# Performance work log

Hardware: AMD Instinct MI355X
Metric: run time of the kernel (lower is better)

## Reference

```python
import jax, jax.numpy as jnp
import numpy as np

N, E = 50000, 800000
IN_DIM, H0, H1, OUT_DIM = 64, 64, 64, 8
NUM_RELS, NUM_BASES = 16, 8


def setup_inputs() -> dict:
    key = jax.random.key(0)
    ks = jax.random.split(key, 20)
    features = jax.random.normal(ks[0], (N, IN_DIM), dtype=jnp.float32)
    etypes = jax.random.randint(ks[1], (E,), 0, NUM_RELS)
    src = jax.random.randint(ks[2], (E,), 0, N)
    dst = jax.random.randint(ks[3], (E,), 0, N)
    # degree normalization 1/in_degree(dst), as DGL stores in g.edata['norm']
    deg = jax.ops.segment_sum(jnp.ones((E,), jnp.float32), dst, num_segments=N)
    norm = (1.0 / jnp.maximum(deg, 1.0))[dst][:, None]  # [E,1]

    def glorot(k, shape):
        fan_in, fan_out = shape[-2], shape[-1]
        lim = jnp.sqrt(6.0 / (fan_in + fan_out)).astype(jnp.float32)
        return jax.random.uniform(k, shape, jnp.float32, -lim, lim)

    dims = [(IN_DIM, H0), (H0, H1), (H1, OUT_DIM)]
    inp = {"features": features, "norm": norm}
    for i, (di, do) in enumerate(dims):
        inp[f"basis{i}"] = glorot(ks[4 + 4 * i], (NUM_BASES, di, do))
        inp[f"comp{i}"] = glorot(ks[5 + 4 * i], (NUM_RELS, NUM_BASES))
        inp[f"loop{i}"] = glorot(ks[6 + 4 * i], (di, do))
        inp[f"bias{i}"] = jnp.zeros((do,), jnp.float32)
    inp["etypes"] = etypes
    inp["src"] = src
    inp["dst"] = dst
    return inp


def rel_graph_conv(h, basis, comp, loop_w, bias, etypes, src, dst, norm, act):
    # basis-decomposed relation weights: [R, din, dout]
    W = jnp.einsum('rb,bio->rio', comp, basis)
    # transform every node under every relation: [N, R, dout]
    h_trans = jnp.einsum('ni,rio->nro', h, W)
    # per-edge gather of (src node, edge relation), degree-normalized
    msg = h_trans[src, etypes] * norm  # [E, dout]
    agg = jax.ops.segment_sum(msg, dst, num_segments=h.shape[0])  # [N, dout]
    out = agg + h @ loop_w + bias  # self-loop + bias (DGL defaults)
    return act(out)


def reference(features, norm, basis0, comp0, loop0, bias0, basis1, comp1, loop1,
              bias1, basis2, comp2, loop2, bias2, etypes, src, dst):
    lrelu = lambda x: jax.nn.leaky_relu(x, negative_slope=0.01)
    h = rel_graph_conv(features, basis0, comp0, loop0, bias0, etypes, src, dst, norm, lrelu)
    h = rel_graph_conv(h, basis1, comp1, loop1, bias1, etypes, src, dst, norm, lrelu)
    h = rel_graph_conv(h, basis2, comp2, loop2, bias2, etypes, src, dst, norm, jax.nn.relu)
    return h
```

## Files before the change

kernel.cpp:

```cpp
#include <hip/hip_runtime.h>

#define NN 50000
#define NE 800000
#define CAP 64
#define KC 72

typedef __bf16 bf16x8 __attribute__((ext_vector_type(8)));
typedef float f32x4 __attribute__((ext_vector_type(4)));
typedef unsigned short ushort;
typedef unsigned int uint;

__device__ inline ushort f2bf(float x) {
  uint u = __builtin_bit_cast(uint, x);
  u += 0x7FFF + ((u >> 16) & 1);
  return (ushort)(u >> 16);
}
__device__ inline float bf2f(ushort u) {
  return __builtin_bit_cast(float, (uint)u << 16);
}


__device__ inline void wprep_body(const float* __restrict__ basis,
                                  const float* __restrict__ loopw,
                                  ushort* __restrict__ W2, int DOUT, int NCOLS,
                                  int idx) {
  int total = KC * NCOLS * 8;
  if (idx >= total) return;
  int j = idx & 7;
  int n = (idx >> 3) % NCOLS;
  int kc = idx / (8 * NCOLS);
  int k = kc * 8 + j;
  float v = 0.f;
  if (n < DOUT) v = (k < 512) ? basis[k * DOUT + n] : loopw[(k - 512) * DOUT + n];
  W2[((size_t)kc * NCOLS + n) * 8 + j] = f2bf(v);
}

__global__ __launch_bounds__(256) void build_kernel(
    const int* __restrict__ dstv, const int* __restrict__ srcv,
    const int* __restrict__ etv, int* __restrict__ cursor, int* __restrict__ pk,
    const float* __restrict__ f, ushort* __restrict__ fb,
    const float* __restrict__ b0, const float* __restrict__ l0, ushort* __restrict__ W0,
    const float* __restrict__ b1, const float* __restrict__ l1, ushort* __restrict__ W1,
    const float* __restrict__ b2, const float* __restrict__ l2, ushort* __restrict__ W2) {
  int blk = blockIdx.x;
  int tid = threadIdx.x;
  if (blk < 3125) {
    int i = blk * 256 + tid;
    int d = dstv[i];
    int p = atomicAdd(&cursor[d], 1);
    if (p < CAP) pk[d * CAP + p] = (etv[i] << 16) | srcv[i];
  } else if (blk < 6250) {
    int i = (blk - 3125) * 256 + tid;
    float4 v = ((const float4*)f)[i];
    ushort4 u;
    u.x = f2bf(v.x); u.y = f2bf(v.y); u.z = f2bf(v.z); u.w = f2bf(v.w);
    ((ushort4*)fb)[i] = u;
  } else if (blk < 6394) {
    wprep_body(b0, l0, W0, 64, 64, (blk - 6250) * 256 + tid);
  } else if (blk < 6538) {
    wprep_body(b1, l1, W1, 64, 64, (blk - 6394) * 256 + tid);
  } else {
    wprep_body(b2, l2, W2, 8, 16, (blk - 6538) * 256 + tid);
  }
}


template <int DOUT, int NCOLS, bool OBF>
__global__ __launch_bounds__(1024, 8) void layer_kernel(
    const ushort* __restrict__ hb,
    const float* __restrict__ comp,
    const int* __restrict__ degv,
    const int* __restrict__ pk,
    const ushort* __restrict__ W2,
    const float* __restrict__ bias,
    void* __restrict__ outp,
    float slope)
{
  __shared__ ushort X[KC][16][8];
  int tid = threadIdx.x;
  int wave = tid >> 6;
  int lane = tid & 63;
  int dbase = blockIdx.x * 16;
  int d = __builtin_amdgcn_readfirstlane(dbase + wave);

  int deg = degv[d];
  int dw = deg > CAP ? CAP : deg;
  const int* pb = pk + (size_t)d * CAP;
  const int4* p4 = (const int4*)pb;
  int ng = dw >> 2;

  float acc[8] = {0.f, 0.f, 0.f, 0.f, 0.f, 0.f, 0.f, 0.f};
  if (ng > 0) {
    int4 pv = p4[0];
    for (int g = 0; g < ng; ++g) {
      int4 nv = pv;
      if (g + 1 < ng) nv = p4[g + 1];
      {
        int pe = __builtin_amdgcn_readfirstlane(pv.x);
        float hv = bf2f(hb[(size_t)(pe & 0xFFFF) * 64 + lane]);
        const float* c = comp + (pe >> 16) * 8;
#pragma unroll
        for (int b = 0; b < 8; ++b) acc[b] = fmaf(c[b], hv, acc[b]);
      }
      {
        int pe = __builtin_amdgcn_readfirstlane(pv.y);
        float hv = bf2f(hb[(size_t)(pe & 0xFFFF) * 64 + lane]);
        const float* c = comp + (pe >> 16) * 8;
#pragma unroll
        for (int b = 0; b < 8; ++b) acc[b] = fmaf(c[b], hv, acc[b]);
      }
      {
        int pe = __builtin_amdgcn_readfirstlane(pv.z);
        float hv = bf2f(hb[(size_t)(pe & 0xFFFF) * 64 + lane]);
        const float* c = comp + (pe >> 16) * 8;
#pragma unroll
        for (int b = 0; b < 8; ++b) acc[b] = fmaf(c[b], hv, acc[b]);
      }
      {
        int pe = __builtin_amdgcn_readfirstlane(pv.w);
        float hv = bf2f(hb[(size_t)(pe & 0xFFFF) * 64 + lane]);
        const float* c = comp + (pe >> 16) * 8;
#pragma unroll
        for (int b = 0; b < 8; ++b) acc[b] = fmaf(c[b], hv, acc[b]);
      }
      pv = nv;
    }
  }
  for (int j = dw & ~3; j < dw; ++j) {
    int pe = __builtin_amdgcn_readfirstlane(pb[j]);
    float hv = bf2f(hb[(size_t)(pe & 0xFFFF) * 64 + lane]);
    const float* c = comp + (pe >> 16) * 8;
#pragma unroll
    for (int b = 0; b < 8; ++b) acc[b] = fmaf(c[b], hv, acc[b]);
  }

  float inv = 1.0f / (float)(deg > 1 ? deg : 1);
  int jj = lane & 7;
  int csub = lane >> 3;
#pragma unroll
  for (int b = 0; b < 8; ++b) X[b * 8 + csub][wave][jj] = f2bf(acc[b] * inv);
  X[64 + csub][wave][jj] = hb[(size_t)d * 64 + lane];
  __syncthreads();

  if (wave < (DOUT == 64 ? 4 : 1)) {
    int q = lane >> 4;
    int r = lane & 15;
    f32x4 acc2 = {0.f, 0.f, 0.f, 0.f};
#pragma unroll
    for (int ks = 0; ks < 18; ++ks) {
      int kc = ks * 4 + q;
      bf16x8 bfrag = *(const bf16x8*)&X[kc][r][0];
      bf16x8 afrag = *(const bf16x8*)(W2 + ((size_t)kc * NCOLS + wave * 16 + r) * 8);
      acc2 = __builtin_amdgcn_mfma_f32_16x16x32_bf16(afrag, bfrag, acc2, 0, 0, 0);
    }
    int m = dbase + r;
    int nb = wave * 16 + q * 4;
    if (nb < DOUT) {
      float4 bv = *(const float4*)(bias + nb);
      float v0 = acc2[0] + bv.x;
      float v1 = acc2[1] + bv.y;
      float v2 = acc2[2] + bv.z;
      float v3 = acc2[3] + bv.w;
      v0 = v0 > 0.f ? v0 : slope * v0;
      v1 = v1 > 0.f ? v1 : slope * v1;
      v2 = v2 > 0.f ? v2 : slope * v2;
      v3 = v3 > 0.f ? v3 : slope * v3;
      if (OBF) {
        ushort4 u;
        u.x = f2bf(v0); u.y = f2bf(v1); u.z = f2bf(v2); u.w = f2bf(v3);
        *(ushort4*)((ushort*)outp + (size_t)m * DOUT + nb) = u;
      } else {
        *(float4*)((float*)outp + (size_t)m * DOUT + nb) = float4{v0, v1, v2, v3};
      }
    }
  }
}


extern "C" void kernel_launch(void* const* d_in, const int* in_sizes, int n_in,
                              void* d_out, int out_size, void* d_ws, size_t ws_size,
                              hipStream_t stream) {
  const float* features = (const float*)d_in[0];
  const float* basis0   = (const float*)d_in[2];
  const float* comp0    = (const float*)d_in[3];
  const float* loop0    = (const float*)d_in[4];
  const float* bias0    = (const float*)d_in[5];
  const float* basis1   = (const float*)d_in[6];
  const float* comp1    = (const float*)d_in[7];
  const float* loop1    = (const float*)d_in[8];
  const float* bias1    = (const float*)d_in[9];
  const float* basis2   = (const float*)d_in[10];
  const float* comp2    = (const float*)d_in[11];
  const float* loop2    = (const float*)d_in[12];
  const float* bias2    = (const float*)d_in[13];
  const int* etypes     = (const int*)d_in[14];
  const int* srcv       = (const int*)d_in[15];
  const int* dstv       = (const int*)d_in[16];

  char* ws = (char*)d_ws;
  size_t off = 0;
  auto alloc = [&](size_t bytes) {
    void* p = ws + off;
    off += (bytes + 255) & ~(size_t)255;
    return p;
  };
  int* cnt      = (int*)alloc(NN * sizeof(int));
  int* pk       = (int*)alloc((size_t)NN * CAP * sizeof(int));
  ushort* W2_0  = (ushort*)alloc((size_t)KC * 64 * 8 * sizeof(ushort));
  ushort* W2_1  = (ushort*)alloc((size_t)KC * 64 * 8 * sizeof(ushort));
  ushort* W2_2  = (ushort*)alloc((size_t)KC * 16 * 8 * sizeof(ushort));
  ushort* fbf   = (ushort*)alloc((size_t)NN * 64 * sizeof(ushort));
  ushort* hA    = (ushort*)alloc((size_t)NN * 64 * sizeof(ushort));
  ushort* hB    = (ushort*)alloc((size_t)NN * 64 * sizeof(ushort));

  hipMemsetAsync(cnt, 0, NN * sizeof(int), stream);
  build_kernel<<<6574, 256, 0, stream>>>(dstv, srcv, etypes, cnt, pk,
                                         features, fbf,
                                         basis0, loop0, W2_0,
                                         basis1, loop1, W2_1,
                                         basis2, loop2, W2_2);

  layer_kernel<64, 64, true><<<3125, 1024, 0, stream>>>(
      fbf, comp0, cnt, pk, W2_0, bias0, hA, 0.01f);
  layer_kernel<64, 64, true><<<3125, 1024, 0, stream>>>(
      hA, comp1, cnt, pk, W2_1, bias1, hB, 0.01f);
  layer_kernel<8, 16, false><<<3125, 1024, 0, stream>>>(
      hB, comp2, cnt, pk, W2_2, bias2, d_out, 0.0f);
}
```

Before: 171.4 us.

## Pad degree counters, batch edge gathers by 16 with zero-coefficient padding

Degree counters move to a stride of 16 ints so each node's counter sits on its own cache line during atomic edge bucketing. The per-edge gather loop becomes a fully unrolled batch of 16 edge loads with branch-free masking, so more independent gathers can be in flight. Edges past the degree point at an extra zero row in a padded relation-coefficient table, which the build kernel now fills. In exchange the counter array and its memset grow 16x, and low-degree nodes gather wasted dummy rows (node 0).

Result: slower. 192.2 us (+12.2%).

```diff
diff --git a/kernel.cpp b/kernel.cpp
--- a/kernel.cpp
+++ b/kernel.cpp
@@ -4,6 +4,7 @@
 #define NE 800000
 #define CAP 64
 #define KC 72
+#define CSTR 16
 
 typedef __bf16 bf16x8 __attribute__((ext_vector_type(8)));
 typedef float f32x4 __attribute__((ext_vector_type(4)));
@@ -41,13 +42,15 @@
     const float* __restrict__ f, ushort* __restrict__ fb,
     const float* __restrict__ b0, const float* __restrict__ l0, ushort* __restrict__ W0,
     const float* __restrict__ b1, const float* __restrict__ l1, ushort* __restrict__ W1,
-    const float* __restrict__ b2, const float* __restrict__ l2, ushort* __restrict__ W2) {
+    const float* __restrict__ b2, const float* __restrict__ l2, ushort* __restrict__ W2,
+    const float* __restrict__ c0, const float* __restrict__ c1,
+    const float* __restrict__ c2, float* __restrict__ cp) {
   int blk = blockIdx.x;
   int tid = threadIdx.x;
   if (blk < 3125) {
     int i = blk * 256 + tid;
     int d = dstv[i];
-    int p = atomicAdd(&cursor[d], 1);
+    int p = atomicAdd(&cursor[(size_t)d * CSTR], 1);
     if (p < CAP) pk[d * CAP + p] = (etv[i] << 16) | srcv[i];
   } else if (blk < 6250) {
     int i = (blk - 3125) * 256 + tid;
@@ -59,8 +62,15 @@
     wprep_body(b0, l0, W0, 64, 64, (blk - 6250) * 256 + tid);
   } else if (blk < 6538) {
     wprep_body(b1, l1, W1, 64, 64, (blk - 6394) * 256 + tid);
+  } else if (blk < 6574) {
+    wprep_body(b2, l2, W2, 8, 16, (blk - 6538) * 256 + tid);
   } else {
-    wprep_body(b2, l2, W2, 8, 16, (blk - 6538) * 256 + tid);
+    int idx = (blk - 6574) * 256 + tid;
+    if (idx < 408) {
+      int l = idx / 136, k = idx % 136;
+      const float* src = (l == 0) ? c0 : ((l == 1) ? c1 : c2);
+      cp[idx] = (k < 128) ? src[k] : 0.f;
+    }
   }
 }
 
@@ -68,7 +78,7 @@
 template <int DOUT, int NCOLS, bool OBF>
 __global__ __launch_bounds__(1024, 8) void layer_kernel(
     const ushort* __restrict__ hb,
-    const float* __restrict__ comp,
+    const float* __restrict__ cpad,
     const int* __restrict__ degv,
     const int* __restrict__ pk,
     const ushort* __restrict__ W2,
@@ -83,55 +93,28 @@
   int dbase = blockIdx.x * 16;
   int d = __builtin_amdgcn_readfirstlane(dbase + wave);
 
-  int deg = degv[d];
+  int deg = degv[(size_t)d * CSTR];
   int dw = deg > CAP ? CAP : deg;
-  const int* pb = pk + (size_t)d * CAP;
-  const int4* p4 = (const int4*)pb;
-  int ng = dw >> 2;
+  const int4* p4 = (const int4*)(pk + (size_t)d * CAP);
 
   float acc[8] = {0.f, 0.f, 0.f, 0.f, 0.f, 0.f, 0.f, 0.f};
-  if (ng > 0) {
-    int4 pv = p4[0];
-    for (int g = 0; g < ng; ++g) {
-      int4 nv = pv;
-      if (g + 1 < ng) nv = p4[g + 1];
-      {
-        int pe = __builtin_amdgcn_readfirstlane(pv.x);
-        float hv = bf2f(hb[(size_t)(pe & 0xFFFF) * 64 + lane]);
-        const float* c = comp + (pe >> 16) * 8;
-#pragma unroll
-        for (int b = 0; b < 8; ++b) acc[b] = fmaf(c[b], hv, acc[b]);
-      }
-      {
-        int pe = __builtin_amdgcn_readfirstlane(pv.y);
-        float hv = bf2f(hb[(size_t)(pe & 0xFFFF) * 64 + lane]);
-        const float* c = comp + (pe >> 16) * 8;
-#pragma unroll
-        for (int b = 0; b < 8; ++b) acc[b] = fmaf(c[b], hv, acc[b]);
-      }
-      {
-        int pe = __builtin_amdgcn_readfirstlane(pv.z);
-        float hv = bf2f(hb[(size_t)(pe & 0xFFFF) * 64 + lane]);
-        const float* c = comp + (pe >> 16) * 8;
-#pragma unroll
-        for (int b = 0; b < 8; ++b) acc[b] = fmaf(c[b], hv, acc[b]);
-      }
-      {
-        int pe = __builtin_amdgcn_readfirstlane(pv.w);
-        float hv = bf2f(hb[(size_t)(pe & 0xFFFF) * 64 + lane]);
-        const float* c = comp + (pe >> 16) * 8;
-#pragma unroll
-        for (int b = 0; b < 8; ++b) acc[b] = fmaf(c[b], hv, acc[b]);
-      }
-      pv = nv;
-    }
-  }
-  for (int j = dw & ~3; j < dw; ++j) {
-    int pe = __builtin_amdgcn_readfirstlane(pb[j]);
-    float hv = bf2f(hb[(size_t)(pe & 0xFFFF) * 64 + lane]);
-    const float* c = comp + (pe >> 16) * 8;
-#pragma unroll
-    for (int b = 0; b < 8; ++b) acc[b] = fmaf(c[b], hv, acc[b]);
+  for (int base = 0; base < dw; base += 16) {
+    int qg = base >> 2;
+    int4 e0 = p4[qg + 0];
+    int4 e1 = p4[qg + 1];
+    int4 e2 = p4[qg + 2];
+    int4 e3 = p4[qg + 3];
+    int pe[16] = {e0.x, e0.y, e0.z, e0.w, e1.x, e1.y, e1.z, e1.w,
+                  e2.x, e2.y, e2.z, e2.w, e3.x, e3.y, e3.z, e3.w};
+#pragma unroll
+    for (int i = 0; i < 16; ++i) {
+      int p = __builtin_amdgcn_readfirstlane(pe[i]);
+      p = (base + i < dw) ? p : (16 << 16);
+      float hv = bf2f(hb[(size_t)(p & 0xFFFF) * 64 + lane]);
+      const float* c = cpad + (p >> 16) * 8;
+#pragma unroll
+      for (int b = 0; b < 8; ++b) acc[b] = fmaf(c[b], hv, acc[b]);
+    }
   }
 
   float inv = 1.0f / (float)(deg > 1 ? deg : 1);
@@ -204,26 +187,28 @@
     off += (bytes + 255) & ~(size_t)255;
     return p;
   };
-  int* cnt      = (int*)alloc(NN * sizeof(int));
+  int* cnt      = (int*)alloc((size_t)NN * CSTR * sizeof(int));
   int* pk       = (int*)alloc((size_t)NN * CAP * sizeof(int));
   ushort* W2_0  = (ushort*)alloc((size_t)KC * 64 * 8 * sizeof(ushort));
   ushort* W2_1  = (ushort*)alloc((size_t)KC * 64 * 8 * sizeof(ushort));
   ushort* W2_2  = (ushort*)alloc((size_t)KC * 16 * 8 * sizeof(ushort));
+  float* cpad   = (float*)alloc(3 * 136 * sizeof(float));
   ushort* fbf   = (ushort*)alloc((size_t)NN * 64 * sizeof(ushort));
   ushort* hA    = (ushort*)alloc((size_t)NN * 64 * sizeof(ushort));
   ushort* hB    = (ushort*)alloc((size_t)NN * 64 * sizeof(ushort));
 
-  hipMemsetAsync(cnt, 0, NN * sizeof(int), stream);
-  build_kernel<<<6574, 256, 0, stream>>>(dstv, srcv, etypes, cnt, pk,
+  hipMemsetAsync(cnt, 0, (size_t)NN * CSTR * sizeof(int), stream);
+  build_kernel<<<6576, 256, 0, stream>>>(dstv, srcv, etypes, cnt, pk,
                                          features, fbf,
                                          basis0, loop0, W2_0,
                                          basis1, loop1, W2_1,
-                                         basis2, loop2, W2_2);
+                                         basis2, loop2, W2_2,
+                                         comp0, comp1, comp2, cpad);
 
   layer_kernel<64, 64, true><<<3125, 1024, 0, stream>>>(
-      fbf, comp0, cnt, pk, W2_0, bias0, hA, 0.01f);
+      fbf, cpad + 0 * 136, cnt, pk, W2_0, bias0, hA, 0.01f);
   layer_kernel<64, 64, true><<<3125, 1024, 0, stream>>>(
-      hA, comp1, cnt, pk, W2_1, bias1, hB, 0.01f);
+      hA, cpad + 1 * 136, cnt, pk, W2_1, bias1, hB, 0.01f);
   layer_kernel<8, 16, false><<<3125, 1024, 0, stream>>>(
-      hB, comp2, cnt, pk, W2_2, bias2, d_out, 0.0f);
-}
+      hB, cpad + 2 * 136, cnt, pk, W2_2, bias2, d_out, 0.0f);
+}
```
